# Optimization experiments

Measured on AMD Instinct MI355X. Metric: run time of the kernel, lower is better.

## Reference

```python
import jax, jax.numpy as jnp
import numpy as np


def conv2d(x, w, stride=1, padding=0, dilation=1):
    return jax.lax.conv_general_dilated(
        x, w, (stride, stride), [(padding, padding), (padding, padding)],
        rhs_dilation=(dilation, dilation),
        dimension_numbers=("NCHW", "OIHW", "NCHW"))


def pixel_shuffle(x, r):
    b, C, h, w = x.shape
    c = C // (r * r)
    x = x.reshape(b, c, r, r, h, w)
    x = x.transpose(0, 1, 4, 2, 5, 3)  # b,c,h,r,w,r
    return x.reshape(b, c, h * r, w * r)


def phitphi(x, PhiW, PhiTW, B):
    N = B * B
    outs = []
    for c in range(3):
        phi = conv2d(x[:, c:c + 1], PhiW[:, c:c + 1], stride=B)  # [b,M,h/B,w/B]
        outs.append(conv2d(phi, PhiTW[c * N:(c + 1) * N]))        # [b,N,h/B,w/B]
    temp = jnp.concatenate(outs, axis=1)  # [b,3N,h/B,w/B]
    return pixel_shuffle(temp, B)


def adconv(data, W, para):
    # Faithful to ADConv: route each output channel to dilation argmax(para[c]),
    # output channels grouped by dilation (stable order within a group), each
    # group scaled by mean(para[group, i]) + 1.
    C, T = para.shape
    indexs = jnp.argmax(para, axis=1)              # softmax preserves argmax
    perm = jnp.argsort(indexs)                     # stable: group channels by dilation
    ys = jnp.stack([conv2d(data, W, padding=i + 1, dilation=i + 1)
                    for i in range(T)], axis=0)    # [T,b,C,H,W]
    mask = jax.nn.one_hot(indexs, T, dtype=para.dtype)  # [C,T]
    cnt = jnp.maximum(mask.sum(0), 1.0)
    mul = (para * mask).sum(0) / cnt + 1.0         # [T]
    d = indexs[perm]                               # dilation per output channel
    sel = ys[d, :, perm]                           # [C,b,H,W]
    sel = sel * mul[d][:, None, None, None]
    return sel.transpose(1, 0, 2, 3)               # [b,C,H,W]


def setup_inputs() -> dict:
    key = jax.random.key(0)
    ks = jax.random.split(key, 32)
    B, M, C, H, W, F = 32, 256, 3, 320, 320, 32
    N = B * B
    bsz = 4
    inp = {
        "xprev": jax.random.normal(ks[0], (bsz, C, H, W), jnp.float32),
        "x": jax.random.normal(ks[1], (bsz, C, H, W), jnp.float32),
        "PhiWeight": jax.random.normal(ks[2], (M, C, B, B), jnp.float32) / B,
        "PhiTWeight": jax.random.normal(ks[3], (3 * N, M, 1, 1), jnp.float32) / B,
        "PhiTb": jax.random.normal(ks[4], (bsz, C, H, W), jnp.float32),
        "lambda_step": jnp.float32(0.5),
        "soft_thr": jnp.float32(0.01),
        "t": jnp.float32(1.0),
        "mergeScale": jnp.float32(1.0),
        "conv_D": jax.random.normal(ks[5], (F, 3, 3, 3), jnp.float32) * 0.08,
        "conv3_G": jax.random.normal(ks[6], (3, F, 3, 3), jnp.float32) * 0.08,
        "c1f_w": jax.random.normal(ks[7], (F, F, 3, 3), jnp.float32) * 0.06,
        "c1f_p": jax.random.normal(ks[8], (F, 1), jnp.float32),
        "c2f_w": jax.random.normal(ks[9], (F, F, 3, 3), jnp.float32) * 0.06,
        "c2f_p": jax.random.normal(ks[10], (F, 3), jnp.float32),
        "c1b_w": jax.random.normal(ks[11], (F, F, 3, 3), jnp.float32) * 0.06,
        "c1b_p": jax.random.normal(ks[12], (F, 1), jnp.float32),
        "c2b_w": jax.random.normal(ks[13], (F, F, 3, 3), jnp.float32) * 0.06,
        "c2b_p": jax.random.normal(ks[14], (F, 3), jnp.float32),
        "c1g_w": jax.random.normal(ks[15], (F, F, 3, 3), jnp.float32) * 0.06,
        "c1g_p": jax.random.normal(ks[16], (F, 1), jnp.float32),
        "c2g_w": jax.random.normal(ks[17], (F, F, 3, 3), jnp.float32) * 0.06,
        "c2g_p": jax.random.normal(ks[18], (F, 3), jnp.float32),
        "BLOCK_SIZE": 32,
    }
    return inp


def reference(xprev, x, PhiWeight, PhiTWeight, PhiTb,
              lambda_step, soft_thr, t, mergeScale,
              conv_D, conv3_G,
              c1f_w, c1f_p, c2f_w, c2f_p,
              c1b_w, c1b_p, c2b_w, c2b_p,
              c1g_w, c1g_p, c2g_w, c2g_p,
              BLOCK_SIZE):
    tplus = (1.0 + jnp.sqrt(1.0 + 4.0 * t * t)) / 2.0
    xi = (t - 1.0) / tplus
    deltax = x - xprev
    zeta = x - lambda_step * phitphi(x, PhiWeight, PhiTWeight, BLOCK_SIZE)
    zeta = zeta - lambda_step * xi * phitphi(deltax, PhiWeight, PhiTWeight, BLOCK_SIZE)
    zeta = zeta + xi * deltax + lambda_step * PhiTb
    x_input = zeta

    x_D = conv2d(x_input, conv_D, padding=1)
    h = jax.nn.relu(adconv(x_D, c1f_w, c1f_p))
    x_forward = adconv(h, c2f_w, c2f_p)
    # soft threshold
    xs = jnp.sign(x_forward) * jax.nn.relu(jnp.abs(x_forward) - soft_thr)
    h = jax.nn.relu(adconv(xs, c1f_w, c1f_p))  # source reuses conv1_forward here
    x_backward = adconv(h, c2b_w, c2b_p)
    h = adconv(jax.nn.relu(x_backward), c1g_w, c1g_p)
    h = adconv(jax.nn.relu(h), c2g_w, c2g_p)
    x_G = conv2d(h, conv3_G, padding=1)
    x_pred = x_input + x_G * mergeScale

    h = jax.nn.relu(adconv(x_forward, c1b_w, c1b_p))
    x_D_est = adconv(h, c2b_w, c2b_p)
    symloss = x_D_est - x_D
    return (x_pred, symloss)
```

## Files before the change

### kernel.cpp

```cpp
#include <hip/hip_runtime.h>
#include <math.h>

#define HW 320
#define IMGSZ (HW*HW)
#define NB 4

typedef __bf16 bf16x8 __attribute__((ext_vector_type(8)));
typedef float  f32x4  __attribute__((ext_vector_type(4)));

__device__ __forceinline__ float4 ld4(const float* p){ return *reinterpret_cast<const float4*>(p); }

__device__ __forceinline__ unsigned short f2b(float f){
  unsigned u = __float_as_uint(f);
  unsigned r = (u + 0x7fffu + ((u>>16)&1u)) >> 16;
  return (unsigned short)r;
}

__global__ void meta_kernel(const float* p0,const float* p1,const float* p2,
                            const float* p3,const float* p4,const float* p5,
                            int* msrc,int* md,float* mscale,int* pres){
  if (threadIdx.x != 0) return;
  int set = blockIdx.x;
  const float* ps[6] = {p0,p1,p2,p3,p4,p5};
  const int Ts[6] = {1,3,1,3,1,3};
  const float* para = ps[set];
  int T = Ts[set];
  int idx[32]; float mx[32];
  for (int c=0;c<32;c++){
    int best=0; float bv=para[c*T];
    for (int t=1;t<T;t++){ float v=para[c*T+t]; if (v>bv){bv=v;best=t;} }
    idx[c]=best; mx[c]=bv;
  }
  float sum[3]={0.f,0.f,0.f}; int cnt[3]={0,0,0};
  for (int c=0;c<32;c++){ sum[idx[c]] += mx[c]; cnt[idx[c]]++; }
  float mul[3];
  for (int t=0;t<3;t++) mul[t] = sum[t]/fmaxf((float)cnt[t],1.f)+1.f;
  int off[3]; off[0]=0; off[1]=cnt[0]; off[2]=cnt[0]+cnt[1];
  int perm[32];
  for (int c=0;c<32;c++) perm[off[idx[c]]++] = c;
  int pb = 0;
  for (int k=0;k<32;k++){
    int s = perm[k];
    msrc[set*32+k]=s; md[set*32+k]=idx[s]+1; mscale[set*32+k]=mul[idx[s]];
    pb |= 1 << (idx[s]+1);
  }
  pres[set] = pb;
}

__global__ void ew_u(const float* __restrict__ x, const float* __restrict__ xprev,
                     const float* __restrict__ t_p, float* __restrict__ u, int n4){
  int i = blockIdx.x*blockDim.x + threadIdx.x;
  if (i >= n4) return;
  float t = *t_p;
  float tplus = (1.f + sqrtf(1.f + 4.f*t*t)) * 0.5f;
  float xi = (t - 1.f)/tplus;
  float4 xv = ld4(x + 4*i); float4 pv = ld4(xprev + 4*i);
  float4 r;
  r.x = xv.x + xi*(xv.x-pv.x);
  r.y = xv.y + xi*(xv.y-pv.y);
  r.z = xv.z + xi*(xv.z-pv.z);
  r.w = xv.w + xi*(xv.w-pv.w);
  *reinterpret_cast<float4*>(u + 4*i) = r;
}


__global__ void pack_phib(const float* __restrict__ PhiW, uint4* __restrict__ PhiB){
  int idx = blockIdx.x*256 + threadIdx.x;
  int lane = idx & 63;
  int t2 = idx >> 6;
  int nf = t2 & 3, ks = (t2>>2)&31, cm = t2>>7;
  int m = (cm&3)*64 + nf*16 + (lane&15);
  int c = cm>>2;
  int kbase = ks*32 + (lane>>4)*8;
  const float* src = PhiW + ((size_t)m*3 + c)*1024 + kbase;
  float4 v0 = ld4(src), v1 = ld4(src+4);
  float vals[8] = {v0.x,v0.y,v0.z,v0.w,v1.x,v1.y,v1.z,v1.w};
  uint4 hi, lo; unsigned* hw = (unsigned*)&hi; unsigned* lw = (unsigned*)&lo;
  #pragma unroll
  for (int p=0;p<4;p++){
    unsigned h0 = f2b(vals[2*p]), h1 = f2b(vals[2*p+1]);
    float r0 = vals[2*p]   - __uint_as_float(h0<<16);
    float r1 = vals[2*p+1] - __uint_as_float(h1<<16);
    hw[p] = h0 | (h1<<16);
    lw[p] = (unsigned)f2b(r0) | ((unsigned)f2b(r1)<<16);
  }
  PhiB[(size_t)t2*128 + lane] = hi;
  PhiB[(size_t)t2*128 + 64 + lane] = lo;
}

__global__ void pack_phitb(const float* __restrict__ PhiTW, uint4* __restrict__ PhiTB){
  int idx = blockIdx.x*256 + threadIdx.x;
  int lane = idx & 63;
  int t2 = idx >> 6;
  int nf = t2 & 3, ks = (t2>>2)&7, cn = t2>>5;
  int n = (cn&15)*64 + nf*16 + (lane&15);
  int c = cn>>4;
  int kbase = ks*32 + (lane>>4)*8;
  const float* src = PhiTW + ((size_t)c*1024 + n)*256 + kbase;
  float4 v0 = ld4(src), v1 = ld4(src+4);
  float vals[8] = {v0.x,v0.y,v0.z,v0.w,v1.x,v1.y,v1.z,v1.w};
  uint4 hi, lo; unsigned* hw = (unsigned*)&hi; unsigned* lw = (unsigned*)&lo;
  #pragma unroll
  for (int p=0;p<4;p++){
    unsigned h0 = f2b(vals[2*p]), h1 = f2b(vals[2*p+1]);
    float r0 = vals[2*p]   - __uint_as_float(h0<<16);
    float r1 = vals[2*p+1] - __uint_as_float(h1<<16);
    hw[p] = h0 | (h1<<16);
    lw[p] = (unsigned)f2b(r0) | ((unsigned)f2b(r1)<<16);
  }
  PhiTB[(size_t)t2*128 + lane] = hi;
  PhiTB[(size_t)t2*128 + 64 + lane] = lo;
}

__global__ __launch_bounds__(256)
void phi_gemm(const float* __restrict__ u, const uint4* __restrict__ PhiB,
              uint4* __restrict__ PhA){
  __shared__ uint4 As[2][2048];
  const int rt = blockIdx.x, mt = blockIdx.y, c = blockIdx.z;
  const int tid = threadIdx.x, lane = tid & 63, w = tid >> 6;

  for (int idx = tid; idx < 4096; idx += 256){
    int m = idx >> 8;
    int f4 = idx & 255;
    int k = f4*4;
    int r = rt*16 + m;
    int b = r/100, blk = r - b*100;
    int bh = blk/10, bw = blk - bh*10;
    int ip = k >> 5, jp = k & 31;
    float4 v = ld4(u + ((size_t)((b*3+c)*HW + bh*32+ip))*HW + bw*32 + jp);
    float vv[4] = {v.x,v.y,v.z,v.w};
    unsigned hh[4], ll[4];
    #pragma unroll
    for (int e=0;e<4;e++){
      hh[e] = f2b(vv[e]);
      ll[e] = f2b(vv[e] - __uint_as_float(hh[e]<<16));
    }
    int kb = k >> 3, off = (k & 7) ? 1 : 0;
    ((uint2*)&As[0][kb*16+m])[off] = make_uint2(hh[0]|(hh[1]<<16), hh[2]|(hh[3]<<16));
    ((uint2*)&As[1][kb*16+m])[off] = make_uint2(ll[0]|(ll[1]<<16), ll[2]|(ll[3]<<16));
  }
  __syncthreads();

  f32x4 acc[4] = {};
  const uint4* bbase = PhiB + (size_t)(c*4+mt)*32*512;
  for (int ksl = 0; ksl < 8; ++ksl){
    int ks = w*8 + ksl;
    bf16x8 ah = __builtin_bit_cast(bf16x8, As[0][ks*64 + lane]);
    bf16x8 al = __builtin_bit_cast(bf16x8, As[1][ks*64 + lane]);
    #pragma unroll
    for (int nf=0; nf<4; ++nf){
      const uint4* bp = bbase + ((size_t)ks*4 + nf)*128;
      bf16x8 bh = __builtin_bit_cast(bf16x8, bp[lane]);
      bf16x8 bl = __builtin_bit_cast(bf16x8, bp[64 + lane]);
      acc[nf] = __builtin_amdgcn_mfma_f32_16x16x32_bf16(ah, bh, acc[nf], 0,0,0);
      acc[nf] = __builtin_amdgcn_mfma_f32_16x16x32_bf16(ah, bl, acc[nf], 0,0,0);
      acc[nf] = __builtin_amdgcn_mfma_f32_16x16x32_bf16(al, bh, acc[nf], 0,0,0);
    }
  }

  __syncthreads();
  float* rf = (float*)As;
  #pragma unroll
  for (int nf=0; nf<4; ++nf)
    ((float4*)rf)[(w*64+lane)*4 + nf] = *(float4*)&acc[nf];
  __syncthreads();

  int o = tid*4;
  int i = o >> 6, j = o & 63;
  int nf = j >> 4, q = i >> 2, reg = i & 3;
  unsigned hh[4], ll[4];
  #pragma unroll
  for (int e=0;e<4;e++){
    int ls = q*16 + (j&15) + e;
    float v = rf[(0*64+ls)*16 + nf*4+reg] + rf[(1*64+ls)*16 + nf*4+reg]
            + rf[(2*64+ls)*16 + nf*4+reg] + rf[(3*64+ls)*16 + nf*4+reg];
    hh[e] = f2b(v);
    ll[e] = f2b(v - __uint_as_float(hh[e]<<16));
  }
  int kb = mt*8 + (j>>3);
  int off = (j & 7) ? 1 : 0;
  ((uint2*)&PhA[((size_t)(0*3+c)*25 + rt)*512 + kb*16 + i])[off] =
      make_uint2(hh[0]|(hh[1]<<16), hh[2]|(hh[3]<<16));
  ((uint2*)&PhA[((size_t)(1*3+c)*25 + rt)*512 + kb*16 + i])[off] =
      make_uint2(ll[0]|(ll[1]<<16), ll[2]|(ll[3]<<16));
}

__global__ __launch_bounds__(256)
void phit_gemm(const uint4* __restrict__ PhA, const uint4* __restrict__ PhiTB,
               const float* __restrict__ u, const float* __restrict__ PhiTb,
               const float* __restrict__ lam_p, float* __restrict__ x_input){
  const int rt = blockIdx.x, nt4 = blockIdx.y, c = blockIdx.z;
  const int tid = threadIdx.x, lane = tid & 63, w = tid >> 6;
  f32x4 acc[4] = {};
  const uint4* ah_base = PhA + ((size_t)(0*3+c)*25 + rt)*512;
  const uint4* al_base = PhA + ((size_t)(1*3+c)*25 + rt)*512;
  const uint4* bbase = PhiTB + (size_t)(c*16 + nt4*4 + w)*8*512;
  #pragma unroll
  for (int ks=0; ks<8; ++ks){
    bf16x8 ah = __builtin_bit_cast(bf16x8, ah_base[ks*64 + lane]);
    bf16x8 al = __builtin_bit_cast(bf16x8, al_base[ks*64 + lane]);
    #pragma unroll
    for (int nf=0; nf<4; ++nf){
      const uint4* bp = bbase + ((size_t)ks*4 + nf)*128;
      bf16x8 bh = __builtin_bit_cast(bf16x8, bp[lane]);
      bf16x8 bl = __builtin_bit_cast(bf16x8, bp[64 + lane]);
      acc[nf] = __builtin_amdgcn_mfma_f32_16x16x32_bf16(ah, bh, acc[nf], 0,0,0);
      acc[nf] = __builtin_amdgcn_mfma_f32_16x16x32_bf16(ah, bl, acc[nf], 0,0,0);
      acc[nf] = __builtin_amdgcn_mfma_f32_16x16x32_bf16(al, bh, acc[nf], 0,0,0);
    }
  }
  float lam = *lam_p;
  int q = lane >> 4, jl = lane & 15;
  #pragma unroll
  for (int nf=0; nf<4; ++nf){
    int n = nt4*256 + w*64 + nf*16 + jl;
    int ip = n >> 5, jp = n & 31;
    #pragma unroll
    for (int reg=0; reg<4; ++reg){
      int r = rt*16 + q*4 + reg;
      int b = r/100, blk = r - b*100;
      int bh_ = blk/10, bw_ = blk - bh_*10;
      size_t g = ((size_t)((b*3+c)*HW + bh_*32+ip))*HW + bw_*32 + jp;
      x_input[g] = u[g] - lam*acc[nf][reg] + lam*PhiTb[g];
    }
  }
}

template<int CIN, int COUT, int NK, int D>
__global__ __launch_bounds__(256)
void conv_direct(const float* __restrict__ in, const float* __restrict__ wts,
                 float* __restrict__ out){
  const int kg = blockIdx.x;
  const int b  = blockIdx.z;
  const int k0 = kg*NK;
  const int tile = blockIdx.y;

  __shared__ float wsm[NK*CIN*12];
  int tid = threadIdx.y*16 + threadIdx.x;
  for (int q = tid; q < NK*CIN*9; q += 256){
    int kk = q/(CIN*9); int rem = q - kk*(CIN*9);
    wsm[(kk*CIN + rem/9)*12 + rem%9] = wts[(size_t)(k0+kk)*(CIN*9) + rem];
  }
  __syncthreads();

  const int x0 = (tile%5)*64 + threadIdx.x*4;
  const int y0 = (tile/5)*32 + threadIdx.y*2;
  float acc[NK][2][4] = {};

  for (int ic=0; ic<CIN; ++ic){
    const float* ip = in + (size_t)(b*CIN+ic)*IMGSZ;
    float wk[NK][9];
    #pragma unroll
    for (int kk=0;kk<NK;kk++){
      #pragma unroll
      for (int q=0;q<9;q++) wk[kk][q] = wsm[(kk*CIN+ic)*12+q];
    }
    #pragma unroll
    for (int r=0; r<2+2*D; ++r){
      int yr = y0 - D + r;
      if (yr < 0 || yr >= HW) continue;
      const float* rp = ip + (size_t)yr*HW;
      float4 v0 = (x0 >= 4)   ? ld4(rp + x0-4) : float4{0.f,0.f,0.f,0.f};
      float4 v1 = ld4(rp + x0);
      float4 v2 = (x0+4 < HW) ? ld4(rp + x0+4) : float4{0.f,0.f,0.f,0.f};
      float w12[12] = {v0.x,v0.y,v0.z,v0.w, v1.x,v1.y,v1.z,v1.w, v2.x,v2.y,v2.z,v2.w};
      #pragma unroll
      for (int kk=0;kk<NK;kk++){
        #pragma unroll
        for (int ky=0; ky<3; ++ky){
          int j = r - ky*D;
          if (j >= 0 && j < 2){
            #pragma unroll
            for (int p=0;p<4;p++){
              #pragma unroll
              for (int kx=0;kx<3;kx++)
                acc[kk][j][p] += wk[kk][ky*3+kx] * w12[4 + p + (kx-1)*D];
            }
          }
        }
      }
    }
  }
  #pragma unroll
  for (int kk=0;kk<NK;kk++){
    int k = k0+kk;
    #pragma unroll
    for (int j=0;j<2;j++){
      size_t oidx = ((size_t)(b*COUT + k)*HW + (y0+j))*HW + x0;
      float4 o; float* op = (float*)&o;
      #pragma unroll
      for (int p=0;p<4;p++) op[p] = acc[kk][j][p];
      *reinterpret_cast<float4*>(out + oidx) = o;
    }
  }
}

__global__ void cvt_blocked(const float* __restrict__ src, uint4* __restrict__ dst){
  int idx = blockIdx.x*256 + threadIdx.x;
  if (idx >= 4*4*320*80) return;
  int x4 = idx % 80; int t = idx / 80;
  int y = t % 320; t /= 320;
  int g = t % 4; int b = t / 4;
  int x = x4*4;
  float vals[8][4];
  #pragma unroll
  for (int c=0;c<8;c++){
    float4 v = ld4(src + (((size_t)(b*32 + g*8 + c)*HW + y)*HW + x));
    vals[c][0]=v.x; vals[c][1]=v.y; vals[c][2]=v.z; vals[c][3]=v.w;
  }
  #pragma unroll
  for (int p=0;p<4;p++){
    uint4 o;
    unsigned* ow = (unsigned*)&o;
    #pragma unroll
    for (int c=0;c<4;c++)
      ow[c] = (unsigned)f2b(vals[2*c][p]) | ((unsigned)f2b(vals[2*c+1][p])<<16);
    dst[(((size_t)(b*4+g)*HW + y)*HW + x + p)] = o;
  }
}

__global__ void pack_w(const float* w0,const float* w1,const float* w2,
                       const float* w3,const float* w4,const float* w5,
                       const float* w6,
                       const int* msrc,const int* md,const float* mscale,
                       uint4* __restrict__ wp){
  const float* wsel[7] = {w0,w1,w2,w3,w4,w5,w6};
  const int set_of[13]  = {0,1,1,1,2,3,3,3,4,5,5,5,6};
  const int cls_of[13]  = {1,1,2,3,1,1,2,3,1,1,2,3,1};
  int slot = blockIdx.x;
  int set = set_of[slot], cls = cls_of[slot];
  const float* W = wsel[set];
  unsigned short* out = (unsigned short*)(wp + (size_t)slot*1152);
  for (int v = threadIdx.x; v < 9216; v += 256){
    int j = v & 7;
    int lane = (v >> 3) & 63;
    int rest = v >> 9;
    int t = rest % 9, h = rest / 9;
    int ocl = lane & 15, q = lane >> 4;
    int oc = h*16 + ocl;
    int ic = q*8 + j;
    float val = 0.f;
    if (set == 6){
      if (oc < 3) val = W[(size_t)oc*(32*9) + ic*9 + t];
    } else {
      if (md[set*32+oc] == cls){
        int src = msrc[set*32+oc];
        val = W[(size_t)src*(32*9) + ic*9 + t] * mscale[set*32+oc];
      }
    }
    out[v] = f2b(val);
  }
}

template<int H,int NPASS,int NH,int ROWS,int ITRANS,int EPI>
__device__ __forceinline__ void conv_body(char* smem,
    const uint4* __restrict__ inb, const uint4* __restrict__ wp,
    void* __restrict__ outp, const int* __restrict__ pres_p, int set,
    const float* __restrict__ thr_p, const float* __restrict__ epi_f32,
    const float* __restrict__ ms_p, int tx, int ty, int b){
  constexpr int TW = 32 + 2*H, TH = ROWS + 2*H, TP = TW*TH;
  constexpr int RPW = ROWS/4;
  constexpr int MT  = ROWS/2;
  constexpr int PW  = ROWS*8;

  const int x0 = tx*32, y0 = ty*ROWS;
  const int tid = threadIdx.x;
  const int lane = tid & 63, w = tid >> 6;
  const int m = lane & 15, q = lane >> 4;

  float thr = (ITRANS==2) ? *thr_p : 0.f;
  uint4* sm16 = (uint4*)smem;
  constexpr int TOT = 4*TP;
  constexpr int NSTG = (TOT + 255)/256;
  for (int base = 0; base < NSTG; base += 4){
    uint4 v[4];
    #pragma unroll
    for (int uu=0; uu<4; ++uu){
      v[uu] = make_uint4(0,0,0,0);
      if (base+uu < NSTG){
        int i = tid + (base+uu)*256;
        if (i < TOT){
          int g = i / TP; int rr = i - g*TP; int r = rr / TW; int c = rr - r*TW;
          int gy = y0 - H + r, gx = x0 - H + c;
          if (gy>=0 && gy<HW && gx>=0 && gx<HW)
            v[uu] = inb[(((size_t)(b*4+g)*HW + gy)*HW + gx)];
        }
      }
    }
    #pragma unroll
    for (int uu=0; uu<4; ++uu){
      if (base+uu < NSTG){
        int i = tid + (base+uu)*256;
        if (i < TOT){
          uint4 vv = v[uu];
          if (ITRANS==1){
            unsigned* pw = (unsigned*)&vv;
            #pragma unroll
            for (int z=0;z<4;z++){
              unsigned lo = pw[z] & 0xffffu, hi = pw[z] >> 16;
              if (lo & 0x8000u) lo = 0;
              if (hi & 0x8000u) hi = 0;
              pw[z] = lo | (hi<<16);
            }
          } else if (ITRANS==2){
            unsigned* pw = (unsigned*)&vv;
            #pragma unroll
            for (int z=0;z<4;z++){
              unsigned lo = pw[z] & 0xffffu, hi = pw[z] >> 16;
              float f0 = __uint_as_float(lo<<16), f1 = __uint_as_float(hi<<16);
              float a0 = fabsf(f0)-thr, a1 = fabsf(f1)-thr;
              f0 = (a0>0.f)? copysignf(a0,f0) : 0.f;
              f1 = (a1>0.f)? copysignf(a1,f1) : 0.f;
              pw[z] = (unsigned)f2b(f0) | ((unsigned)f2b(f1)<<16);
            }
          }
          sm16[i] = vv;
        }
      }
    }
  }
  __syncthreads();

  f32x4 acc[MT][NH] = {};
  int pres = (NPASS==3) ? pres_p[set] : 2;
  for (int d = 1; d <= NPASS; ++d){
    if (NPASS==3 && !((pres>>d)&1)) continue;
    const uint4* wbase = wp + (size_t)(d-1)*1152;
    bf16x8 bcur[NH];
    #pragma unroll
    for (int h=0; h<NH; ++h)
      bcur[h] = __builtin_bit_cast(bf16x8, wbase[(h*9 + 0)*64 + lane]);
    for (int t = 0; t < 9; ++t){
      bf16x8 bnxt[NH];
      if (t < 8){
        #pragma unroll
        for (int h=0; h<NH; ++h)
          bnxt[h] = __builtin_bit_cast(bf16x8, wbase[(h*9 + t+1)*64 + lane]);
      }
      int dy = (t/3 - 1)*d, dx = (t%3 - 1)*d;
      const uint4* sp = sm16 + q*TP + (H+dy)*TW + H + dx;
      #pragma unroll
      for (int mt=0; mt<MT; ++mt){
        int r = mt >> 1, xh = mt & 1;
        bf16x8 a = __builtin_bit_cast(bf16x8, sp[(w*RPW + r)*TW + xh*16 + m]);
        #pragma unroll
        for (int h=0; h<NH; ++h)
          acc[mt][h] = __builtin_amdgcn_mfma_f32_16x16x32_bf16(a, bcur[h], acc[mt][h], 0,0,0);
      }
      if (t < 8){
        #pragma unroll
        for (int h=0; h<NH; ++h) bcur[h] = bnxt[h];
      }
    }
  }

  if (EPI >= 2){
    float ms = (EPI==2) ? *ms_p : 0.f;
    #pragma unroll
    for (int mt=0; mt<MT; ++mt){
      int r = mt >> 1, xh = mt & 1;
      int y = y0 + w*RPW + r;
      int x = x0 + xh*16 + q*4;
      #pragma unroll
      for (int h=0; h<NH; ++h){
        int oc = h*16 + m;
        if (EPI==2){
          if (oc < 3){
            size_t off = (((size_t)(b*3+oc)*HW + y)*HW + x);
            float4 e = ld4(epi_f32 + off);
            float4 o;
            o.x = e.x + ms*acc[mt][h][0];
            o.y = e.y + ms*acc[mt][h][1];
            o.z = e.z + ms*acc[mt][h][2];
            o.w = e.w + ms*acc[mt][h][3];
            *reinterpret_cast<float4*>((float*)outp + off) = o;
          }
        } else {
          size_t off = (((size_t)(b*32+oc)*HW + y)*HW + x);
          float4 e = ld4(epi_f32 + off);
          float4 o;
          o.x = acc[mt][h][0] - e.x;
          o.y = acc[mt][h][1] - e.y;
          o.z = acc[mt][h][2] - e.z;
          o.w = acc[mt][h][3] - e.w;
          *reinterpret_cast<float4*>((float*)outp + off) = o;
        }
      }
    }
  } else {
    __syncthreads();
    short* sw = (short*)smem + (size_t)w*PW*40;
    #pragma unroll
    for (int mt=0; mt<MT; ++mt){
      int r = mt >> 1, xh = mt & 1;
      #pragma unroll
      for (int h=0; h<NH; ++h){
        int oc = h*16 + m;
        #pragma unroll
        for (int reg=0; reg<4; ++reg){
          float v = acc[mt][h][reg];
          if (EPI==1) v = fmaxf(v, 0.f);
          int P = r*32 + xh*16 + q*4 + reg;
          sw[P*40 + oc] = (short)f2b(v);
        }
      }
    }
    #pragma unroll
    for (int i=0; i<PW/16; ++i){
      int id = i*64 + lane;
      int g2 = id / PW, P = id % PW;
      uint4 val = *reinterpret_cast<uint4*>(&sw[P*40 + g2*8]);
      int y2 = y0 + w*RPW + (P>>5), x2 = x0 + (P&31);
      ((uint4*)outp)[(((size_t)(b*4+g2)*HW + y2)*HW + x2)] = val;
    }
  }
}

template<int H,int NPASS,int NH,int ITRANS,int EPI,int ROWS>
__global__ __launch_bounds__(256, 2)
void mfma_conv_s(const uint4* __restrict__ inb, const uint4* __restrict__ wp,
                 void* __restrict__ outp,
                 const int* __restrict__ pres_p, int set,
                 const float* __restrict__ thr_p,
                 const float* __restrict__ epi_f32,
                 const float* __restrict__ ms_p){
  constexpr int TP = (32+2*H)*(ROWS+2*H);
  constexpr int S1 = 4*TP*16;
  constexpr int S2 = (EPI<=1) ? ROWS*8*40*2*4 : 0;
  constexpr int SB = S1 > S2 ? S1 : S2;
  __shared__ __align__(16) char smem[SB];
  conv_body<H,NPASS,NH,ROWS,ITRANS,EPI>(smem, inb, wp, outp, pres_p, set,
                                        thr_p, epi_f32, ms_p,
                                        blockIdx.x, blockIdx.y, blockIdx.z);
}

template<int H,int NPASS,int NH,int ROWS,int IT0,int EP0,int IT1,int EP1>
__global__ __launch_bounds__(256, 2)
void mfma_conv_d(const uint4* __restrict__ in0, const uint4* __restrict__ in1,
                 const uint4* __restrict__ wp0, const uint4* __restrict__ wp1,
                 void* __restrict__ o0, void* __restrict__ o1,
                 const int* __restrict__ pres_p, int set,
                 const float* __restrict__ thr_p,
                 const float* __restrict__ e0, const float* __restrict__ e1,
                 const float* __restrict__ ms_p){
  constexpr int TP = (32+2*H)*(ROWS+2*H);
  constexpr int S1 = 4*TP*16;
  constexpr int SE = ROWS*8*40*2*4;
  constexpr int S2 = ((EP0<=1)||(EP1<=1)) ? SE : 0;
  constexpr int SB = S1 > S2 ? S1 : S2;
  __shared__ __align__(16) char smem[SB];
  int b = blockIdx.z & 3, job = blockIdx.z >> 2;
  if (job == 0)
    conv_body<H,NPASS,NH,ROWS,IT0,EP0>(smem, in0, wp0, o0, pres_p, set,
                                       thr_p, e0, ms_p, blockIdx.x, blockIdx.y, b);
  else
    conv_body<H,NPASS,NH,ROWS,IT1,EP1>(smem, in1, wp1, o1, pres_p, set,
                                       thr_p, e1, ms_p, blockIdx.x, blockIdx.y, b);
}

extern "C" void kernel_launch(void* const* d_in, const int* in_sizes, int n_in,
                              void* d_out, int out_size, void* d_ws, size_t ws_size,
                              hipStream_t stream) {
  const float* xprev = (const float*)d_in[0];
  const float* x     = (const float*)d_in[1];
  const float* PhiW  = (const float*)d_in[2];
  const float* PhiTW = (const float*)d_in[3];
  const float* PhiTb = (const float*)d_in[4];
  const float* lam   = (const float*)d_in[5];
  const float* sthr  = (const float*)d_in[6];
  const float* t_p   = (const float*)d_in[7];
  const float* mrg   = (const float*)d_in[8];
  const float* convD = (const float*)d_in[9];
  const float* conv3G= (const float*)d_in[10];
  const float* c1f_w=(const float*)d_in[11]; const float* c1f_p=(const float*)d_in[12];
  const float* c2f_w=(const float*)d_in[13]; const float* c2f_p=(const float*)d_in[14];
  const float* c1b_w=(const float*)d_in[15]; const float* c1b_p=(const float*)d_in[16];
  const float* c2b_w=(const float*)d_in[17]; const float* c2b_p=(const float*)d_in[18];
  const float* c1g_w=(const float*)d_in[19]; const float* c1g_p=(const float*)d_in[20];
  const float* c2g_w=(const float*)d_in[21]; const float* c2g_p=(const float*)d_in[22];

  char* ws = (char*)d_ws;
  const size_t BL = (size_t)NB*4*IMGSZ*16;
  uint4* xDb = (uint4*)(ws + 0*BL);
  uint4* Bb  = (uint4*)(ws + 1*BL);
  uint4* Cb  = (uint4*)(ws + 2*BL);
  uint4* Db  = (uint4*)(ws + 3*BL);
  uint4* Eb  = (uint4*)(ws + 4*BL);
  float* xDf = (float*)(ws + 5*BL);
  float* x_input = (float*)(ws + 5*BL + 52428800);
  float* u       = (float*)(ws + 5*BL + 52428800 + 4915200);
  char*  phir    = ws + 5*BL + 52428800 + 2*4915200;
  uint4* PhiB    = (uint4*)phir;
  uint4* PhA     = (uint4*)(phir + 3145728);
  uint4* PhiTB   = (uint4*)xDf;
  uint4* Wp      = (uint4*)(ws + 5*BL + 52428800 + 3*4915200);
  char*  mbase   = ws + 5*BL + 52428800 + 3*4915200 + 13*18432;
  int*   msrc    = (int*)(mbase);
  int*   md      = (int*)(mbase + 768);
  float* mscale  = (float*)(mbase + 2*768);
  int*   pres    = (int*)(mbase + 3*768);

  float* out0 = (float*)d_out;
  float* out1 = out0 + (size_t)NB*3*IMGSZ;

  meta_kernel<<<6, 64, 0, stream>>>(c1f_p,c2f_p,c1b_p,c2b_p,c1g_p,c2g_p,
                                    msrc, md, mscale, pres);
  pack_w<<<13, 256, 0, stream>>>(c1f_w,c2f_w,c1b_w,c2b_w,c1g_w,c2g_w,conv3G,
                                 msrc, md, mscale, Wp);
  pack_phib<<<384, 256, 0, stream>>>(PhiW, PhiB);
  pack_phitb<<<384, 256, 0, stream>>>(PhiTW, PhiTB);

  ew_u<<<1200, 256, 0, stream>>>(x, xprev, t_p, u, 307200);
  phi_gemm<<<dim3(25,4,3), 256, 0, stream>>>(u, PhiB, PhA);
  phit_gemm<<<dim3(25,4,3), 256, 0, stream>>>(PhA, PhiTB, u, PhiTb, lam, x_input);

  conv_direct<3,32,2,1><<<dim3(16,50,NB), dim3(16,16), 0, stream>>>(x_input, convD, xDf);
  cvt_blocked<<<1600, 256, 0, stream>>>(xDf, xDb);

  dim3 mg(10,40,NB);
  dim3 mg2(10,40,NB*2);
  uint4* W_c1f = Wp + 0*1152;
  uint4* W_c2f = Wp + 1*1152;
  uint4* W_c1b = Wp + 4*1152;
  uint4* W_c2b = Wp + 5*1152;
  uint4* W_c1g = Wp + 8*1152;
  uint4* W_c2g = Wp + 9*1152;
  uint4* W_g3  = Wp + 12*1152;

  mfma_conv_s<1,1,2,0,1,8><<<mg,256,0,stream>>>(xDb, W_c1f, Bb, nullptr,0, nullptr,nullptr,nullptr);
  mfma_conv_s<3,3,2,0,0,8><<<mg,256,0,stream>>>(Bb, W_c2f, Cb, pres,1, nullptr,nullptr,nullptr);
  mfma_conv_d<1,1,2,8, 2,1, 0,1><<<mg2,256,0,stream>>>(Cb, Cb, W_c1f, W_c1b, Db, Bb,
                                                       nullptr,0, sthr, nullptr,nullptr, nullptr);
  mfma_conv_d<3,3,2,8, 0,0, 0,3><<<mg2,256,0,stream>>>(Db, Bb, W_c2b, W_c2b, Eb, out1,
                                                       pres,3, nullptr, nullptr, xDf, nullptr);
  mfma_conv_s<1,1,2,1,0,8><<<mg,256,0,stream>>>(Eb, W_c1g, Db, nullptr,0, nullptr,nullptr,nullptr);
  mfma_conv_s<3,3,2,1,0,8><<<mg,256,0,stream>>>(Db, W_c2g, Eb, pres,5, nullptr,nullptr,nullptr);
  mfma_conv_s<1,1,1,0,2,8><<<mg,256,0,stream>>>(Eb, W_g3, out0, nullptr,0, nullptr, x_input, mrg);
}
```

Before: 440.1 us.

## Fuse conv_D with bf16 blocked conversion and read symloss epilogue from bf16

Replaces the fp32 direct conv_D kernel plus the separate fp32-to-bf16 blocked conversion with a single shared-memory-tiled kernel that writes the bf16 channel-blocked layout directly. The symloss epilogue now reads x_D from that bf16 blocked buffer instead of the fp32 copy, which removes the fp32 intermediate write and read. The MFMA weight prefetch is also changed to a two-deep ring. The cost is lower precision in the symloss subtraction, since x_D is now rounded to bf16.

```diff
diff --git a/kernel.cpp b/kernel.cpp
--- a/kernel.cpp
+++ b/kernel.cpp
@@ -226,97 +226,43 @@
   }
 }
 
-template<int CIN, int COUT, int NK, int D>
 __global__ __launch_bounds__(256)
-void conv_direct(const float* __restrict__ in, const float* __restrict__ wts,
-                 float* __restrict__ out){
-  const int kg = blockIdx.x;
-  const int b  = blockIdx.z;
-  const int k0 = kg*NK;
-  const int tile = blockIdx.y;
-
-  __shared__ float wsm[NK*CIN*12];
-  int tid = threadIdx.y*16 + threadIdx.x;
-  for (int q = tid; q < NK*CIN*9; q += 256){
-    int kk = q/(CIN*9); int rem = q - kk*(CIN*9);
-    wsm[(kk*CIN + rem/9)*12 + rem%9] = wts[(size_t)(k0+kk)*(CIN*9) + rem];
-  }
+void conv_direct_blocked(const float* __restrict__ in, const float* __restrict__ wts,
+                         uint4* __restrict__ dst){
+  const int tile = blockIdx.x, g = blockIdx.y, b = blockIdx.z;
+  const int x0 = (tile % 20)*16, y0 = (tile / 20)*16;
+  const int tid = threadIdx.x;
+  __shared__ float ism[3*18*20];
+  __shared__ float wsm[8*27];
+  for (int i = tid; i < 3*18*18; i += 256){
+    int ic = i / 324; int rr = i - ic*324; int r = rr/18, c = rr - r*18;
+    int gy = y0 - 1 + r, gx = x0 - 1 + c;
+    float v = 0.f;
+    if (gy>=0 && gy<HW && gx>=0 && gx<HW)
+      v = in[(size_t)(b*3+ic)*IMGSZ + (size_t)gy*HW + gx];
+    ism[(ic*18+r)*20 + c] = v;
+  }
+  if (tid < 216) wsm[tid] = wts[(size_t)(g*8 + tid/27)*27 + (tid%27)];
   __syncthreads();
 
-  const int x0 = (tile%5)*64 + threadIdx.x*4;
-  const int y0 = (tile/5)*32 + threadIdx.y*2;
-  float acc[NK][2][4] = {};
-
-  for (int ic=0; ic<CIN; ++ic){
-    const float* ip = in + (size_t)(b*CIN+ic)*IMGSZ;
-    float wk[NK][9];
-    #pragma unroll
-    for (int kk=0;kk<NK;kk++){
+  const int px = tid & 15, py = tid >> 4;
+  float acc[8] = {};
+  #pragma unroll
+  for (int ic=0; ic<3; ++ic)
+    #pragma unroll
+    for (int ky=0; ky<3; ++ky)
       #pragma unroll
-      for (int q=0;q<9;q++) wk[kk][q] = wsm[(kk*CIN+ic)*12+q];
-    }
-    #pragma unroll
-    for (int r=0; r<2+2*D; ++r){
-      int yr = y0 - D + r;
-      if (yr < 0 || yr >= HW) continue;
-      const float* rp = ip + (size_t)yr*HW;
-      float4 v0 = (x0 >= 4)   ? ld4(rp + x0-4) : float4{0.f,0.f,0.f,0.f};
-      float4 v1 = ld4(rp + x0);
-      float4 v2 = (x0+4 < HW) ? ld4(rp + x0+4) : float4{0.f,0.f,0.f,0.f};
-      float w12[12] = {v0.x,v0.y,v0.z,v0.w, v1.x,v1.y,v1.z,v1.w, v2.x,v2.y,v2.z,v2.w};
-      #pragma unroll
-      for (int kk=0;kk<NK;kk++){
+      for (int kx=0; kx<3; ++kx){
+        float v = ism[(ic*18+py+ky)*20 + px+kx];
         #pragma unroll
-        for (int ky=0; ky<3; ++ky){
-          int j = r - ky*D;
-          if (j >= 0 && j < 2){
-            #pragma unroll
-            for (int p=0;p<4;p++){
-              #pragma unroll
-              for (int kx=0;kx<3;kx++)
-                acc[kk][j][p] += wk[kk][ky*3+kx] * w12[4 + p + (kx-1)*D];
-            }
-          }
-        }
-      }
-    }
-  }
-  #pragma unroll
-  for (int kk=0;kk<NK;kk++){
-    int k = k0+kk;
-    #pragma unroll
-    for (int j=0;j<2;j++){
-      size_t oidx = ((size_t)(b*COUT + k)*HW + (y0+j))*HW + x0;
-      float4 o; float* op = (float*)&o;
-      #pragma unroll
-      for (int p=0;p<4;p++) op[p] = acc[kk][j][p];
-      *reinterpret_cast<float4*>(out + oidx) = o;
-    }
-  }
-}
-
-__global__ void cvt_blocked(const float* __restrict__ src, uint4* __restrict__ dst){
-  int idx = blockIdx.x*256 + threadIdx.x;
-  if (idx >= 4*4*320*80) return;
-  int x4 = idx % 80; int t = idx / 80;
-  int y = t % 320; t /= 320;
-  int g = t % 4; int b = t / 4;
-  int x = x4*4;
-  float vals[8][4];
-  #pragma unroll
-  for (int c=0;c<8;c++){
-    float4 v = ld4(src + (((size_t)(b*32 + g*8 + c)*HW + y)*HW + x));
-    vals[c][0]=v.x; vals[c][1]=v.y; vals[c][2]=v.z; vals[c][3]=v.w;
-  }
-  #pragma unroll
-  for (int p=0;p<4;p++){
-    uint4 o;
-    unsigned* ow = (unsigned*)&o;
-    #pragma unroll
-    for (int c=0;c<4;c++)
-      ow[c] = (unsigned)f2b(vals[2*c][p]) | ((unsigned)f2b(vals[2*c+1][p])<<16);
-    dst[(((size_t)(b*4+g)*HW + y)*HW + x + p)] = o;
-  }
+        for (int o=0;o<8;o++)
+          acc[o] += wsm[o*27 + ic*9 + ky*3 + kx] * v;
+      }
+  uint4 ov; unsigned* ow = (unsigned*)&ov;
+  #pragma unroll
+  for (int p=0;p<4;p++)
+    ow[p] = (unsigned)f2b(acc[2*p]) | ((unsigned)f2b(acc[2*p+1])<<16);
+  dst[(((size_t)(b*4+g)*HW + (y0+py))*HW + x0+px)] = ov;
 }
 
 __global__ void pack_w(const float* w0,const float* w1,const float* w2,
@@ -356,7 +302,7 @@
 __device__ __forceinline__ void conv_body(char* smem,
     const uint4* __restrict__ inb, const uint4* __restrict__ wp,
     void* __restrict__ outp, const int* __restrict__ pres_p, int set,
-    const float* __restrict__ thr_p, const float* __restrict__ epi_f32,
+    const float* __restrict__ thr_p, const float* __restrict__ epi_ptr,
     const float* __restrict__ ms_p, int tx, int ty, int b){
   constexpr int TW = 32 + 2*H, TH = ROWS + 2*H, TP = TW*TH;
   constexpr int RPW = ROWS/4;
@@ -426,16 +372,20 @@
   for (int d = 1; d <= NPASS; ++d){
     if (NPASS==3 && !((pres>>d)&1)) continue;
     const uint4* wbase = wp + (size_t)(d-1)*1152;
-    bf16x8 bcur[NH];
-    #pragma unroll
-    for (int h=0; h<NH; ++h)
-      bcur[h] = __builtin_bit_cast(bf16x8, wbase[(h*9 + 0)*64 + lane]);
+    bf16x8 pf[2][NH];
+    #pragma unroll
+    for (int h=0; h<NH; ++h){
+      pf[0][h] = __builtin_bit_cast(bf16x8, wbase[(h*9 + 0)*64 + lane]);
+      pf[1][h] = __builtin_bit_cast(bf16x8, wbase[(h*9 + 1)*64 + lane]);
+    }
     for (int t = 0; t < 9; ++t){
-      bf16x8 bnxt[NH];
-      if (t < 8){
+      bf16x8 use[NH];
+      #pragma unroll
+      for (int h=0; h<NH; ++h) use[h] = pf[t&1][h];
+      if (t < 7){
         #pragma unroll
         for (int h=0; h<NH; ++h)
-          bnxt[h] = __builtin_bit_cast(bf16x8, wbase[(h*9 + t+1)*64 + lane]);
+          pf[t&1][h] = __builtin_bit_cast(bf16x8, wbase[(h*9 + t+2)*64 + lane]);
       }
       int dy = (t/3 - 1)*d, dx = (t%3 - 1)*d;
       const uint4* sp = sm16 + q*TP + (H+dy)*TW + H + dx;
@@ -445,11 +395,7 @@
         bf16x8 a = __builtin_bit_cast(bf16x8, sp[(w*RPW + r)*TW + xh*16 + m]);
         #pragma unroll
         for (int h=0; h<NH; ++h)
-          acc[mt][h] = __builtin_amdgcn_mfma_f32_16x16x32_bf16(a, bcur[h], acc[mt][h], 0,0,0);
-      }
-      if (t < 8){
-        #pragma unroll
-        for (int h=0; h<NH; ++h) bcur[h] = bnxt[h];
+          acc[mt][h] = __builtin_amdgcn_mfma_f32_16x16x32_bf16(a, use[h], acc[mt][h], 0,0,0);
       }
     }
   }
@@ -467,7 +413,7 @@
         if (EPI==2){
           if (oc < 3){
             size_t off = (((size_t)(b*3+oc)*HW + y)*HW + x);
-            float4 e = ld4(epi_f32 + off);
+            float4 e = ld4(epi_ptr + off);
             float4 o;
             o.x = e.x + ms*acc[mt][h][0];
             o.y = e.y + ms*acc[mt][h][1];
@@ -476,13 +422,18 @@
             *reinterpret_cast<float4*>((float*)outp + off) = o;
           }
         } else {
+          const uint4* xb = (const uint4*)epi_ptr;
+          int g2 = oc >> 3, ci = oc & 7;
+          size_t bse = (((size_t)(b*4+g2)*HW + y)*HW + x);
+          float4 o; float* op = (float*)&o;
+          #pragma unroll
+          for (int p=0;p<4;p++){
+            uint4 vv = xb[bse + p];
+            unsigned short sh = ((const unsigned short*)&vv)[ci];
+            float e = __uint_as_float(((unsigned)sh)<<16);
+            op[p] = acc[mt][h][p] - e;
+          }
           size_t off = (((size_t)(b*32+oc)*HW + y)*HW + x);
-          float4 e = ld4(epi_f32 + off);
-          float4 o;
-          o.x = acc[mt][h][0] - e.x;
-          o.y = acc[mt][h][1] - e.y;
-          o.z = acc[mt][h][2] - e.z;
-          o.w = acc[mt][h][3] - e.w;
           *reinterpret_cast<float4*>((float*)outp + off) = o;
         }
       }
@@ -522,7 +473,7 @@
                  void* __restrict__ outp,
                  const int* __restrict__ pres_p, int set,
                  const float* __restrict__ thr_p,
-                 const float* __restrict__ epi_f32,
+                 const float* __restrict__ epi_ptr,
                  const float* __restrict__ ms_p){
   constexpr int TP = (32+2*H)*(ROWS+2*H);
   constexpr int S1 = 4*TP*16;
@@ -530,7 +481,7 @@
   constexpr int SB = S1 > S2 ? S1 : S2;
   __shared__ __align__(16) char smem[SB];
   conv_body<H,NPASS,NH,ROWS,ITRANS,EPI>(smem, inb, wp, outp, pres_p, set,
-                                        thr_p, epi_f32, ms_p,
+                                        thr_p, epi_ptr, ms_p,
                                         blockIdx.x, blockIdx.y, blockIdx.z);
 }
 
@@ -614,8 +565,7 @@
   phi_gemm<<<dim3(25,4,3), 256, 0, stream>>>(u, PhiB, PhA);
   phit_gemm<<<dim3(25,4,3), 256, 0, stream>>>(PhA, PhiTB, u, PhiTb, lam, x_input);
 
-  conv_direct<3,32,2,1><<<dim3(16,50,NB), dim3(16,16), 0, stream>>>(x_input, convD, xDf);
-  cvt_blocked<<<1600, 256, 0, stream>>>(xDf, xDb);
+  conv_direct_blocked<<<dim3(400,4,NB), 256, 0, stream>>>(x_input, convD, xDb);
 
   dim3 mg(10,40,NB);
   dim3 mg2(10,40,NB*2);
@@ -632,7 +582,7 @@
   mfma_conv_d<1,1,2,8, 2,1, 0,1><<<mg2,256,0,stream>>>(Cb, Cb, W_c1f, W_c1b, Db, Bb,
                                                        nullptr,0, sthr, nullptr,nullptr, nullptr);
   mfma_conv_d<3,3,2,8, 0,0, 0,3><<<mg2,256,0,stream>>>(Db, Bb, W_c2b, W_c2b, Eb, out1,
-                                                       pres,3, nullptr, nullptr, xDf, nullptr);
+                                                       pres,3, nullptr, nullptr, (const float*)xDb, nullptr);
   mfma_conv_s<1,1,2,1,0,8><<<mg,256,0,stream>>>(Eb, W_c1g, Db, nullptr,0, nullptr,nullptr,nullptr);
   mfma_conv_s<3,3,2,1,0,8><<<mg,256,0,stream>>>(Db, W_c2g, Eb, pres,5, nullptr,nullptr,nullptr);
   mfma_conv_s<1,1,1,0,2,8><<<mg,256,0,stream>>>(Eb, W_g3, out0, nullptr,0, nullptr, x_input, mrg);
```

New measurement: 438.9 us. No clear change (-0.3%).
